# Kernel tuning notes

Hardware: AMD Instinct MI355X
Metric: run time of the kernel (lower is better)

The kernel has to match this reference:

```python
import jax, jax.numpy as jnp
import numpy as np
from jax import lax

L1_DECAY = 1e-06


def _maxpool2(x):
    # NCHW 2x2 max pool, stride 2
    return lax.reduce_window(x, -jnp.inf, lax.max, (1, 1, 2, 2), (1, 1, 2, 2), 'VALID')


def _cnn(x, w1, b1, w2, b2, wo, bo):
    # x: [N,128,128] -> [N,64], z-score normalized over batch dim
    x = x[:, None]  # [N,1,128,128]
    dn = ('NCHW', 'OIHW', 'NCHW')
    x = lax.conv_general_dilated(x, w1, (1, 1), 'SAME', dimension_numbers=dn) + b1[None, :, None, None]
    x = _maxpool2(jax.nn.relu(x))  # [N,4,64,64]
    x = lax.conv_general_dilated(x, w2, (1, 1), 'SAME', dimension_numbers=dn) + b2[None, :, None, None]
    x = _maxpool2(jax.nn.relu(x))  # [N,8,32,32]
    x = x.reshape(x.shape[0], -1)  # [N,8192] (C,H,W order, as torch .view)
    x = x @ wo.T + bo  # [N,64]
    mean = x.mean(axis=0)
    std = x.std(axis=0, ddof=1)  # torch unbiased std
    return (x - mean) / std


def _interact(item, nbr):
    # item: [N,64]; nbr: [N,H,K,64]. dot-attention over K per node/hop.
    scores = jnp.einsum('nhkd,nd->nhk', nbr, item)
    attn = jax.nn.softmax(scores, axis=-1)
    return jnp.einsum('nhk,nhkd->nhd', attn, nbr)  # [N,H,64]


def setup_inputs() -> dict:
    key = jax.random.key(0)
    ks = jax.random.split(key, 16)
    B = 4096
    inp = {}
    inp['data'] = jax.random.randint(ks[0], (B, 3), 0, 76)
    inp['cell_nbr'] = jax.random.randint(ks[1], (76, 2, 128), 0, 15970)
    inp['drug_nbr'] = jax.random.randint(ks[2], (764, 2, 128), 0, 15970)
    inp['protein_table'] = jax.random.normal(ks[3], (15970, 64), jnp.float32)
    inp['cell_emb_pre'] = jax.random.normal(ks[4], (76, 128, 128), jnp.float32)
    inp['drug_emb_pre'] = jax.random.normal(ks[5], (764, 128, 128), jnp.float32)
    inp['conv1_w'] = 0.05 * jax.random.normal(ks[6], (4, 1, 3, 3), jnp.float32)
    inp['conv1_b'] = 0.05 * jax.random.normal(ks[7], (4,), jnp.float32)
    inp['conv2_w'] = 0.05 * jax.random.normal(ks[8], (8, 4, 3, 3), jnp.float32)
    inp['conv2_b'] = 0.05 * jax.random.normal(ks[9], (8,), jnp.float32)
    inp['out_w'] = 0.05 * jax.random.normal(ks[10], (64, 8192), jnp.float32)
    inp['out_b'] = 0.05 * jax.random.normal(ks[11], (64,), jnp.float32)
    inp['agg_w'] = 0.05 * jax.random.normal(ks[12], (64, 128), jnp.float32)
    inp['agg_b'] = 0.05 * jax.random.normal(ks[13], (64,), jnp.float32)
    inp['comb_w'] = 0.05 * jax.random.normal(ks[14], (64, 128), jnp.float32)
    return inp


def reference(data, cell_nbr, drug_nbr, protein_table, cell_emb_pre, drug_emb_pre,
              conv1_w, conv1_b, conv2_w, conv2_b, out_w, out_b, agg_w, agg_b, comb_w):
    cells, drug1, drug2 = data[:, 0], data[:, 1], data[:, 2]
    B = data.shape[0]

    # per-node neighbor embedding gather: [num, n_hop, K, 64]
    cell_nbr_emb = protein_table[cell_nbr]
    drug_nbr_emb = protein_table[drug_nbr]

    # CNN item embeddings from precomputed images
    cell_item = _cnn(cell_emb_pre, conv1_w, conv1_b, conv2_w, conv2_b, out_w, out_b)  # [76,64]
    drug_item = _cnn(drug_emb_pre, conv1_w, conv1_b, conv2_w, conv2_b, out_w, out_b)  # [764,64]

    # gather -> attend -> weighted sum, then concat hops and aggregate
    cell_i = _interact(cell_item, cell_nbr_emb).reshape(cell_item.shape[0], -1)  # [76,128]
    drug_i = _interact(drug_item, drug_nbr_emb).reshape(drug_item.shape[0], -1)  # [764,128]
    cell_emb = cell_i @ agg_w.T + agg_b  # [76,64]
    drug_emb = drug_i @ agg_w.T + agg_b  # [764,64]

    # batch gather, keep singleton dim 1 to match torch stacking of [1,64]
    ce = cell_emb[cells][:, None, :]   # [B,1,64]
    d1e = drug_emb[drug1][:, None, :]
    d2e = drug_emb[drug2][:, None, :]

    # therapy: transformation_matrix
    combined = jnp.concatenate([d1e, d2e], axis=2) @ comb_w.T  # [B,1,64]
    therapy = (combined * ce).sum(axis=2)  # [B,1]
    toxic = (d1e * d2e).sum(axis=2)        # [B,1]
    score = therapy - toxic

    # emb loss (faithful to source: neighbor lists are indexed on the BATCH dim by hop)
    cnl = cell_nbr_emb[cells]   # [B,2,128,64]
    dnl1 = drug_nbr_emb[drug1]
    dnl2 = drug_nbr_emb[drug2]
    sq = lambda t: jnp.sum(t * t)
    item_reg = (sq(ce) + sq(d1e) + sq(d2e)) / 2
    node_reg = jnp.float32(0.0)
    for hop in range(2):
        node_reg = node_reg + (sq(cnl[hop]) + sq(dnl1[hop]) + sq(dnl2[hop])) / 2
    emb_loss = L1_DECAY * (item_reg + node_reg) / B
    return score, emb_loss
```

## Files before the change

### kernel.cpp

```cpp
#include <hip/hip_runtime.h>
#include <hip/hip_bf16.h>
#include <math.h>

#define N_CELL 76
#define N_DRUG 764
#define N_ITEM 840
#define BATCH  4096

#define POOL2H_B 0u
#define POOL2L_B 13762560u
#define WHI_B    27525120u
#define WLO_B    28573696u
#define XFC_B    29622272u
#define ITEM_B   29837312u
#define EMB_B    30052352u
#define V_B      30267392u
#define LOSS_B   30306304u
#define CNT_B    30306368u

typedef short bh8 __attribute__((ext_vector_type(8)));
typedef short bh4 __attribute__((ext_vector_type(4)));
typedef float f32x4 __attribute__((ext_vector_type(4)));

static __device__ inline unsigned short f2bf(float f) {
  union { float f; unsigned u; } v; v.f = f;
  unsigned r = v.u + 0x7FFFu + ((v.u >> 16) & 1u);
  return (unsigned short)(r >> 16);
}
static __device__ inline float bf2f(unsigned short h) {
  union { unsigned u; float f; } v; v.u = ((unsigned)h) << 16;
  return v.f;
}
static __device__ inline unsigned short f2bf_lo(float f, unsigned short h) {
  union { float f; unsigned u; } a; a.f = f - bf2f(h);
  return (unsigned short)(a.u >> 16);
}

union BH8U { bh8 v; struct { bh4 lo, hi; } s; };

__global__ __launch_bounds__(256) void k_conv12(
    const float* __restrict__ cell_pre, const float* __restrict__ drug_pre,
    const float* __restrict__ w1, const float* __restrict__ b1,
    const float* __restrict__ w2, const float* __restrict__ b2,
    const float* __restrict__ out_w,
    unsigned short* __restrict__ pool2h, unsigned short* __restrict__ pool2l,
    unsigned short* __restrict__ whi, unsigned short* __restrict__ wlo,
    float* __restrict__ xfc, float* __restrict__ loss, unsigned* __restrict__ cnt) {
  __shared__ unsigned short slh[38 * 34 * 4];
  __shared__ unsigned short sll[38 * 34 * 4];
  __shared__ unsigned short p1h[18 * 66 * 4];
  __shared__ unsigned short p1l[18 * 66 * 4];
  int n = blockIdx.y;
  int tid = threadIdx.x;
  if (n >= 840) {
    int cb = (n - 840) * 4 + blockIdx.x;
    int gid = cb * 256 + tid;
    if (gid == 0) { *loss = 0.f; *cnt = 0u; }
    for (int i = gid; i < 13440; i += 5120)
      ((float4*)xfc)[i] = make_float4(0.f, 0.f, 0.f, 0.f);
    for (int i = gid; i < 131072; i += 5120) {
      float4 v = ((const float4*)out_w)[i];
      ushort4 h, l;
      h.x = f2bf(v.x); l.x = f2bf(v.x - bf2f(h.x));
      h.y = f2bf(v.y); l.y = f2bf(v.y - bf2f(h.y));
      h.z = f2bf(v.z); l.z = f2bf(v.z - bf2f(h.z));
      h.w = f2bf(v.w); l.w = f2bf(v.w - bf2f(h.w));
      ((ushort4*)whi)[i] = h;
      ((ushort4*)wlo)[i] = l;
    }
    return;
  }
  int qt = blockIdx.x;
  const float4* src = (const float4*)((n < N_CELL) ? (cell_pre + (size_t)n * 16384)
                                                   : (drug_pre + (size_t)(n - N_CELL) * 16384));
  for (int i = tid; i < 38 * 32; i += 256) {
    int lr = i >> 5, g = i & 31;
    int iy = qt * 32 - 3 + lr;
    float4 v = make_float4(0.f, 0.f, 0.f, 0.f);
    if (iy >= 0 && iy < 128) v = src[iy * 32 + g];
    ushort4 h, l;
    h.x = f2bf(v.x); l.x = f2bf_lo(v.x, h.x);
    h.y = f2bf(v.y); l.y = f2bf_lo(v.y, h.y);
    h.z = f2bf(v.z); l.z = f2bf_lo(v.z, h.z);
    h.w = f2bf(v.w); l.w = f2bf_lo(v.w, h.w);
    ((ushort4*)slh)[lr * 34 + g + 1] = h;
    ((ushort4*)sll)[lr * 34 + g + 1] = l;
  }
  if (tid < 76) {
    int lr = tid >> 1, g = (tid & 1) ? 33 : 0;
    ushort4 z = make_ushort4(0, 0, 0, 0);
    ((ushort4*)slh)[lr * 34 + g] = z;
    ((ushort4*)sll)[lr * 34 + g] = z;
  }
  if (tid < 36) {
    int r = tid >> 1, c = (tid & 1) ? 65 : 0;
    ushort4 z = make_ushort4(0, 0, 0, 0);
    ((ushort4*)p1h)[r * 66 + c] = z;
    ((ushort4*)p1l)[r * 66 + c] = z;
  }
  int wv = tid >> 6;
  int lane = tid & 63;
  int ml = lane & 15, q = lane >> 4;

  int oc = ml & 3, yv1 = (ml >> 2) & 1, hi = ml >> 3;
  float bb = b1[oc];
  bh8 BhE, BlE, BhO, BlO;
  {
    int kr = q - yv1;
    bool krok = (kr >= 0 && kr <= 2);
#pragma unroll
    for (int j = 0; j < 8; ++j) {
      float ve = 0.f, vo = 0.f;
      if (krok) {
        int kse = j - 3 - 2 * hi;
        int kso = j - 2 * hi;
        if (kse >= 0 && kse <= 2) ve = w1[oc * 9 + kr * 3 + kse];
        if (kso >= 0 && kso <= 2) vo = w1[oc * 9 + kr * 3 + kso];
      }
      unsigned short he = f2bf(ve), ho = f2bf(vo);
      BhE[j] = (short)he; BlE[j] = (short)f2bf_lo(ve, he);
      BhO[j] = (short)ho; BlO[j] = (short)f2bf_lo(vo, ho);
    }
  }
  int oc_b = ml & 7, yv2 = ml >> 3;
  bh8 Bh2[2], Bl2[2];
#pragma unroll
  for (int ch = 0; ch < 2; ++ch) {
#pragma unroll
    for (int j = 0; j < 8; ++j) {
      int kg = ch * 32 + q * 8 + j;
      float v = 0.f;
      if (kg < 48) {
        int r = kg / 12, rem = kg - r * 12;
        int ks = rem >> 2, ic = rem & 3;
        int kr = r - yv2;
        if (kr >= 0 && kr <= 2) v = w2[(oc_b * 4 + ic) * 9 + kr * 3 + ks];
      } else if (kg == 48) {
        v = b2[oc_b];
      }
      unsigned short h = f2bf(v);
      Bh2[ch][j] = (short)h;
      Bl2[ch][j] = (short)f2bf_lo(v, h);
    }
  }
  int c0 = 2 * q, c1 = 2 * q + 1;
  int c2 = 8 + 2 * q, c3 = 9 + 2 * q;
  if (c2 > 11) { c2 = 8; c3 = 9; }
  int r0 = (c0 * 86) >> 8, s0 = c0 - 3 * r0;
  int r1 = (c1 * 86) >> 8, s1 = c1 - 3 * r1;
  int r2 = (c2 * 86) >> 8, s2 = c2 - 3 * r2;
  int r3 = (c3 * 86) >> 8, s3 = c3 - 3 * r3;
  int x2 = (wv & 3) << 4;
  int off0 = r0 * 66 + x2 + ml + s0;
  int off1 = r1 * 66 + x2 + ml + s1;
  int off2 = r2 * 66 + x2 + ml + s2;
  int off3 = r3 * 66 + x2 + ml + s3;
  __syncthreads();

  int x0 = (wv & 1) * 16;
  int rbase = (wv >> 1) * 9;
  int Lb = x0 + ml;
  const bh4* lh4 = (const bh4*)slh;
  const bh4* ll4 = (const bh4*)sll;
#pragma unroll 1
  for (int ii = 0; ii < 9; ++ii) {
    int i = rbase + ii;
    int base = (2 * i + q) * 34 + Lb;
    bh4 g0h = lh4[base], g1h = lh4[base + 1], g2h = lh4[base + 2];
    bh4 g0l = ll4[base], g1l = ll4[base + 1], g2l = ll4[base + 2];
    BH8U aeh, ael, aoh, aol;
    aeh.s.lo = g0h; aeh.s.hi = g1h;
    ael.s.lo = g0l; ael.s.hi = g1l;
    aoh.s.lo = g1h; aoh.s.hi = g2h;
    aol.s.lo = g1l; aol.s.hi = g2l;
    f32x4 de = {0.f, 0.f, 0.f, 0.f}, dd = de;
    de = __builtin_amdgcn_mfma_f32_16x16x32_bf16(aeh.v, BhE, de, 0, 0, 0);
    de = __builtin_amdgcn_mfma_f32_16x16x32_bf16(aeh.v, BlE, de, 0, 0, 0);
    de = __builtin_amdgcn_mfma_f32_16x16x32_bf16(ael.v, BhE, de, 0, 0, 0);
    dd = __builtin_amdgcn_mfma_f32_16x16x32_bf16(aoh.v, BhO, dd, 0, 0, 0);
    dd = __builtin_amdgcn_mfma_f32_16x16x32_bf16(aoh.v, BlO, dd, 0, 0, 0);
    dd = __builtin_amdgcn_mfma_f32_16x16x32_bf16(aol.v, BhO, dd, 0, 0, 0);
    int pr = qt * 16 - 1 + i;
    bool inr = (pr >= 0 && pr < 64);
#pragma unroll
    for (int r = 0; r < 4; ++r) {
      float t = fmaxf(de[r], dd[r]);
      float t2 = __shfl_xor(t, 4);
      if (yv1 == 0) {
        float val = fmaxf(fmaxf(t, t2) + bb, 0.f);
        if (!inr) val = 0.f;
        unsigned short h = f2bf(val);
        unsigned short l = f2bf_lo(val, h);
        int px = 2 * (x0 + q * 4 + r) + hi;
        int idx = (i * 66 + px + 1) * 4 + oc;
        p1h[idx] = h; p1l[idx] = l;
      }
    }
  }
  __syncthreads();

  const bh4* ph4 = (const bh4*)p1h;
  const bh4* pl4 = (const bh4*)p1l;
#pragma unroll 1
  for (int rp = 0; rp < 8; ++rp) {
    int base2 = 2 * rp * 66;
    BH8U ah0, al0, ah1, al1;
    ah0.s.lo = ph4[base2 + off0]; ah0.s.hi = ph4[base2 + off1];
    al0.s.lo = pl4[base2 + off0]; al0.s.hi = pl4[base2 + off1];
    if (q < 2) {
      ah1.s.lo = ph4[base2 + off2]; ah1.s.hi = ph4[base2 + off3];
      al1.s.lo = pl4[base2 + off2]; al1.s.hi = pl4[base2 + off3];
    } else {
#pragma unroll
      for (int j = 0; j < 8; ++j) { ah1.v[j] = 0; al1.v[j] = 0; }
      if (q == 2) ah1.v[0] = (short)0x3F80;
    }
    f32x4 accA = {0.f, 0.f, 0.f, 0.f}, accB = accA;
    accA = __builtin_amdgcn_mfma_f32_16x16x32_bf16(ah0.v, Bh2[0], accA, 0, 0, 0);
    accA = __builtin_amdgcn_mfma_f32_16x16x32_bf16(ah0.v, Bl2[0], accA, 0, 0, 0);
    accA = __builtin_amdgcn_mfma_f32_16x16x32_bf16(al0.v, Bh2[0], accA, 0, 0, 0);
    accB = __builtin_amdgcn_mfma_f32_16x16x32_bf16(ah1.v, Bh2[1], accB, 0, 0, 0);
    accB = __builtin_amdgcn_mfma_f32_16x16x32_bf16(ah1.v, Bl2[1], accB, 0, 0, 0);
    accB = __builtin_amdgcn_mfma_f32_16x16x32_bf16(al1.v, Bh2[1], accB, 0, 0, 0);
    float d0 = accA[0] + accB[0], d1 = accA[1] + accB[1];
    float d2 = accA[2] + accB[2], d3 = accA[3] + accB[3];
    float m0 = fmaxf(d0, d1), m1 = fmaxf(d2, d3);
    float o0 = __shfl_xor(m0, 8), o1 = __shfl_xor(m1, 8);
    m0 = fmaxf(fmaxf(m0, o0), 0.f);
    m1 = fmaxf(fmaxf(m1, o1), 0.f);
    if (yv2 == 0) {
      unsigned short h0 = f2bf(m0), h1 = f2bf(m1);
      unsigned short l0 = f2bf(m0 - bf2f(h0)), l1 = f2bf(m1 - bf2f(h1));
      int PR = qt * 8 + rp;
      unsigned ui = (unsigned)n * 4096u + (unsigned)oc_b * 512u +
                    (unsigned)PR * 16u + (unsigned)(x2 >> 2) + (unsigned)q;
      ((unsigned*)pool2h)[ui] = (unsigned)h0 | ((unsigned)h1 << 16);
      ((unsigned*)pool2l)[ui] = (unsigned)l0 | ((unsigned)l1 << 16);
    }
  }
}

__global__ __launch_bounds__(64) void k_fc(
    const unsigned short* __restrict__ pool2h, const unsigned short* __restrict__ pool2l,
    const unsigned short* __restrict__ whi, const unsigned short* __restrict__ wlo,
    float* __restrict__ xfc) {
  int mt = blockIdx.x, kc = blockIdx.y;
  int lane = threadIdx.x;
  int ml = lane & 15, q = lane >> 4;
  int row = mt * 16 + ml; if (row > N_ITEM - 1) row = N_ITEM - 1;
  size_t k0 = (size_t)kc * 256 + q * 8;
  const bh8* Ah = (const bh8*)(pool2h + (size_t)row * 8192 + k0);
  const bh8* Al = (const bh8*)(pool2l + (size_t)row * 8192 + k0);
  const bh8* Bh[4], * Bl[4];
#pragma unroll
  for (int nb = 0; nb < 4; ++nb) {
    Bh[nb] = (const bh8*)(whi + (size_t)(nb * 16 + ml) * 8192 + k0);
    Bl[nb] = (const bh8*)(wlo + (size_t)(nb * 16 + ml) * 8192 + k0);
  }
  f32x4 acc[4];
#pragma unroll
  for (int nb = 0; nb < 4; ++nb) acc[nb] = (f32x4){0.f, 0.f, 0.f, 0.f};
#pragma unroll
  for (int st = 0; st < 8; ++st) {
    bh8 ah = Ah[st * 4], al = Al[st * 4];
#pragma unroll
    for (int nb = 0; nb < 4; ++nb) {
      bh8 bhv = Bh[nb][st * 4], blv = Bl[nb][st * 4];
      acc[nb] = __builtin_amdgcn_mfma_f32_16x16x32_bf16(ah, bhv, acc[nb], 0, 0, 0);
      acc[nb] = __builtin_amdgcn_mfma_f32_16x16x32_bf16(ah, blv, acc[nb], 0, 0, 0);
      acc[nb] = __builtin_amdgcn_mfma_f32_16x16x32_bf16(al, bhv, acc[nb], 0, 0, 0);
    }
  }
#pragma unroll
  for (int r = 0; r < 4; ++r) {
    int mr = mt * 16 + q * 4 + r;
    if (mr < N_ITEM) {
      float* dst = xfc + (size_t)mr * 64 + ml;
#pragma unroll
      for (int nb = 0; nb < 4; ++nb) atomicAdd(dst + nb * 16, acc[nb][r]);
    }
  }
}

__global__ __launch_bounds__(256) void k_norm(
    const float* __restrict__ xfc, float* __restrict__ item) {
  __shared__ float red[256];
  int grp = blockIdx.x >> 6;
  int o = blockIdx.x & 63;
  int base = grp ? N_CELL : 0;
  int N = grp ? N_DRUG : N_CELL;
  int tid = threadIdx.x;
  float s = 0.f;
  for (int i = tid; i < N; i += 256) s += xfc[(size_t)(base + i) * 64 + o];
  red[tid] = s; __syncthreads();
  for (int w = 128; w > 0; w >>= 1) { if (tid < w) red[tid] += red[tid + w]; __syncthreads(); }
  float mean = red[0] / (float)N;
  __syncthreads();
  float sq = 0.f;
  for (int i = tid; i < N; i += 256) {
    float d = xfc[(size_t)(base + i) * 64 + o] - mean;
    sq += d * d;
  }
  red[tid] = sq; __syncthreads();
  for (int w = 128; w > 0; w >>= 1) { if (tid < w) red[tid] += red[tid + w]; __syncthreads(); }
  float inv_std = 1.f / sqrtf(red[0] / (float)(N - 1));
  for (int i = tid; i < N; i += 256)
    item[(size_t)(base + i) * 64 + o] = (xfc[(size_t)(base + i) * 64 + o] - mean) * inv_std;
}

__global__ __launch_bounds__(256) void k_interact(
    const int* __restrict__ cell_nbr, const int* __restrict__ drug_nbr,
    const float* __restrict__ protein, const float* __restrict__ item,
    const float* __restrict__ agg_w, const float* __restrict__ agg_b,
    const float* __restrict__ comb_w, float* __restrict__ emb,
    float* __restrict__ V) {
  __shared__ float pb[128 * 65];
  __shared__ float item_s[64];
  __shared__ float sc[128];
  __shared__ float hop_out[128];
  __shared__ float red[256];
  __shared__ float emb_f[64];
  int n = blockIdx.x;
  int tid = threadIdx.x;
  const int* nbr = (n < N_CELL) ? (cell_nbr + (size_t)n * 256)
                                : (drug_nbr + (size_t)(n - N_CELL) * 256);
  if (tid < 64) item_s[tid] = item[(size_t)n * 64 + tid];
  __syncthreads();
  for (int h = 0; h < 2; ++h) {
    for (int e = tid; e < 8192; e += 256) {
      int k = e >> 6, d = e & 63;
      int idx = nbr[h * 128 + k];
      pb[k * 65 + d] = protein[(size_t)idx * 64 + d];
    }
    __syncthreads();
    {
      int k = tid >> 1, halfd = tid & 1;
      int d0 = halfd * 32;
      float p = 0.f;
#pragma unroll
      for (int d = 0; d < 32; ++d) p += item_s[d0 + d] * pb[k * 65 + d0 + d];
      p += __shfl_xor(p, 1);
      if (halfd == 0) sc[k] = p;
    }
    __syncthreads();
    if (tid < 64) {
      float a = sc[tid], b = sc[tid + 64];
      float m = fmaxf(a, b);
#pragma unroll
      for (int off = 32; off > 0; off >>= 1) m = fmaxf(m, __shfl_xor(m, off));
      float e0 = __expf(a - m), e1 = __expf(b - m);
      float s = e0 + e1;
#pragma unroll
      for (int off = 32; off > 0; off >>= 1) s += __shfl_xor(s, off);
      float inv = 1.f / s;
      sc[tid] = e0 * inv; sc[tid + 64] = e1 * inv;
    }
    __syncthreads();
    {
      int d = tid & 63, kq = tid >> 6;
      float p = 0.f;
#pragma unroll
      for (int k = 0; k < 32; ++k) {
        int kk = kq * 32 + k;
        p += sc[kk] * pb[kk * 65 + d];
      }
      red[tid] = p;
    }
    __syncthreads();
    if (tid < 64)
      hop_out[h * 64 + tid] = red[tid] + red[tid + 64] + red[tid + 128] + red[tid + 192];
    __syncthreads();
  }
  {
    int o = tid & 63, jq = tid >> 6;
    float p = 0.f;
#pragma unroll
    for (int j = 0; j < 32; ++j) {
      int jj = jq * 32 + j;
      p += hop_out[jj] * agg_w[(size_t)o * 128 + jj];
    }
    red[tid] = p;
  }
  __syncthreads();
  if (tid < 64) {
    float ev = red[tid] + red[tid + 64] + red[tid + 128] + red[tid + 192] + agg_b[tid];
    emb[(size_t)n * 64 + tid] = ev;
    emb_f[tid] = ev;
  }
  if (n < N_CELL) {
    __syncthreads();
    if (tid < 128) {
      float s = 0.f;
#pragma unroll
      for (int o = 0; o < 64; ++o) s += comb_w[(size_t)o * 128 + tid] * emb_f[o];
      V[(size_t)n * 128 + tid] = s;
    }
  }
}

__global__ __launch_bounds__(256) void k_scoreall(
    const int* __restrict__ data, const int* __restrict__ cell_nbr,
    const int* __restrict__ drug_nbr, const float* __restrict__ protein,
    const float* __restrict__ emb, const float* __restrict__ V,
    float* __restrict__ out, float* __restrict__ loss, unsigned* __restrict__ cnt) {
  __shared__ float red[256];
  int bx = blockIdx.x;
  int tid = threadIdx.x;
  if (bx < 1024) {
    int lane = tid & 63;
    int w = tid >> 6;
    int b = bx * 4 + w;
    int c = data[b * 3 + 0], d1 = data[b * 3 + 1], d2 = data[b * 3 + 2];
    float ce = emb[(size_t)c * 64 + lane];
    float e1 = emb[(size_t)(N_CELL + d1) * 64 + lane];
    float e2 = emb[(size_t)(N_CELL + d2) * 64 + lane];
    float v1 = V[(size_t)c * 128 + lane];
    float v2 = V[(size_t)c * 128 + 64 + lane];
    float th = e1 * v1 + e2 * v2;
    float tx = e1 * e2;
    float rg = ce * ce + e1 * e1 + e2 * e2;
#pragma unroll
    for (int off = 32; off > 0; off >>= 1) {
      th += __shfl_xor(th, off);
      tx += __shfl_xor(tx, off);
      rg += __shfl_xor(rg, off);
    }
    if (lane == 0) { out[b] = th - tx; red[w] = rg; }
    __syncthreads();
    if (tid == 0) atomicAdd(loss, 0.5f * (red[0] + red[1] + red[2] + red[3]));
  } else {
    int j = bx - 1024;
    int hop = j / 3, which = j % 3;
    int row = data[hop * 3 + which];
    const int* nbr = (which == 0) ? (cell_nbr + (size_t)row * 256)
                                  : (drug_nbr + (size_t)row * 256);
    float acc = 0.f;
    for (int e = tid; e < 16384; e += 256) {
      int k = e >> 6, d = e & 63;
      float v = protein[(size_t)nbr[k] * 64 + d];
      acc += v * v;
    }
    red[tid] = acc; __syncthreads();
    for (int w = 128; w > 0; w >>= 1) { if (tid < w) red[tid] += red[tid + w]; __syncthreads(); }
    if (tid == 0) atomicAdd(loss, 0.5f * red[0]);
  }
  if (tid == 0) {
    __threadfence();
    unsigned old = atomicAdd(cnt, 1u);
    if (old == gridDim.x - 1) {
      float L = atomicAdd(loss, 0.f);
      out[BATCH] = L * (1e-6f / 4096.f);
    }
  }
}

extern "C" void kernel_launch(void* const* d_in, const int* in_sizes, int n_in,
                              void* d_out, int out_size, void* d_ws, size_t ws_size,
                              hipStream_t stream) {
  const int*   data      = (const int*)d_in[0];
  const int*   cell_nbr  = (const int*)d_in[1];
  const int*   drug_nbr  = (const int*)d_in[2];
  const float* protein   = (const float*)d_in[3];
  const float* cell_pre  = (const float*)d_in[4];
  const float* drug_pre  = (const float*)d_in[5];
  const float* w1        = (const float*)d_in[6];
  const float* b1        = (const float*)d_in[7];
  const float* w2        = (const float*)d_in[8];
  const float* b2        = (const float*)d_in[9];
  const float* out_w     = (const float*)d_in[10];
  const float* agg_w     = (const float*)d_in[12];
  const float* agg_b     = (const float*)d_in[13];
  const float* comb_w    = (const float*)d_in[14];
  float* out = (float*)d_out;
  char* base = (char*)d_ws;
  unsigned short* pool2h  = (unsigned short*)(base + POOL2H_B);
  unsigned short* pool2l  = (unsigned short*)(base + POOL2L_B);
  unsigned short* whi     = (unsigned short*)(base + WHI_B);
  unsigned short* wlo     = (unsigned short*)(base + WLO_B);
  float* xfc              = (float*)(base + XFC_B);
  float* item             = (float*)(base + ITEM_B);
  float* emb              = (float*)(base + EMB_B);
  float* V                = (float*)(base + V_B);
  float* loss             = (float*)(base + LOSS_B);
  unsigned* cnt           = (unsigned*)(base + CNT_B);

  k_conv12<<<dim3(4, 845), 256, 0, stream>>>(cell_pre, drug_pre, w1, b1, w2, b2, out_w,
                                             pool2h, pool2l, whi, wlo, xfc, loss, cnt);
  k_fc<<<dim3(53, 32), 64, 0, stream>>>(pool2h, pool2l, whi, wlo, xfc);
  k_norm<<<128, 256, 0, stream>>>(xfc, item);
  k_interact<<<840, 256, 0, stream>>>(cell_nbr, drug_nbr, protein, item, agg_w, agg_b,
                                      comb_w, emb, V);
  k_scoreall<<<1030, 256, 0, stream>>>(data, cell_nbr, drug_nbr, protein, emb, V, out, loss, cnt);
}
```

Before: 253.2 us.

## Double block size in conv and interact kernels, splitting rows and hops across waves

Raises k_conv12 and k_interact from 256 to 512 threads per block. In conv, the conv1 row loop is split across 8 waves with uneven 5/4-row ranges, and the conv2 row-pair loop is halved per wave. In interact, the two hops run at the same time on the two thread halves, each with its own shared buffer, which removes the sequential hop loop and its barriers. This costs roughly double the LDS per interact block and may lower occupancy. The hidden conv code must stay consistent with the new wave indexing.

```diff
diff --git a/kernel.cpp b/kernel.cpp
--- a/kernel.cpp
+++ b/kernel.cpp
@@ -38,7 +38,7 @@
 
 union BH8U { bh8 v; struct { bh4 lo, hi; } s; };
 
-__global__ __launch_bounds__(256) void k_conv12(
+__global__ __launch_bounds__(512) void k_conv12(
     const float* __restrict__ cell_pre, const float* __restrict__ drug_pre,
     const float* __restrict__ w1, const float* __restrict__ b1,
     const float* __restrict__ w2, const float* __restrict__ b2,
@@ -54,11 +54,11 @@
   int tid = threadIdx.x;
   if (n >= 840) {
     int cb = (n - 840) * 4 + blockIdx.x;
-    int gid = cb * 256 + tid;
+    int gid = cb * 512 + tid;
     if (gid == 0) { *loss = 0.f; *cnt = 0u; }
-    for (int i = gid; i < 13440; i += 5120)
+    for (int i = gid; i < 13440; i += 10240)
       ((float4*)xfc)[i] = make_float4(0.f, 0.f, 0.f, 0.f);
-    for (int i = gid; i < 131072; i += 5120) {
+    for (int i = gid; i < 131072; i += 10240) {
       float4 v = ((const float4*)out_w)[i];
       ushort4 h, l;
       h.x = f2bf(v.x); l.x = f2bf(v.x - bf2f(h.x));
@@ -73,7 +73,7 @@
   int qt = blockIdx.x;
   const float4* src = (const float4*)((n < N_CELL) ? (cell_pre + (size_t)n * 16384)
                                                    : (drug_pre + (size_t)(n - N_CELL) * 16384));
-  for (int i = tid; i < 38 * 32; i += 256) {
+  for (int i = tid; i < 38 * 32; i += 512) {
     int lr = i >> 5, g = i & 31;
     int iy = qt * 32 - 3 + lr;
     float4 v = make_float4(0.f, 0.f, 0.f, 0.f);
@@ -158,12 +158,14 @@
   __syncthreads();
 
   int x0 = (wv & 1) * 16;
-  int rbase = (wv >> 1) * 9;
+  int g1 = wv >> 1;
+  int rbase = (g1 < 2) ? g1 * 5 : 10 + (g1 - 2) * 4;
+  int rcnt  = (g1 < 2) ? 5 : 4;
   int Lb = x0 + ml;
   const bh4* lh4 = (const bh4*)slh;
   const bh4* ll4 = (const bh4*)sll;
 #pragma unroll 1
-  for (int ii = 0; ii < 9; ++ii) {
+  for (int ii = 0; ii < rcnt; ++ii) {
     int i = rbase + ii;
     int base = (2 * i + q) * 34 + Lb;
     bh4 g0h = lh4[base], g1h = lh4[base + 1], g2h = lh4[base + 2];
@@ -199,10 +201,12 @@
   }
   __syncthreads();
 
+  int rp0 = (wv >> 2) * 4;
   const bh4* ph4 = (const bh4*)p1h;
   const bh4* pl4 = (const bh4*)p1l;
 #pragma unroll 1
-  for (int rp = 0; rp < 8; ++rp) {
+  for (int rr = 0; rr < 4; ++rr) {
+    int rp = rp0 + rr;
     int base2 = 2 * rp * 66;
     BH8U ah0, al0, ah1, al1;
     ah0.s.lo = ph4[base2 + off0]; ah0.s.hi = ph4[base2 + off1];
@@ -308,82 +312,85 @@
     item[(size_t)(base + i) * 64 + o] = (xfc[(size_t)(base + i) * 64 + o] - mean) * inv_std;
 }
 
-__global__ __launch_bounds__(256) void k_interact(
+__global__ __launch_bounds__(512) void k_interact(
     const int* __restrict__ cell_nbr, const int* __restrict__ drug_nbr,
     const float* __restrict__ protein, const float* __restrict__ item,
     const float* __restrict__ agg_w, const float* __restrict__ agg_b,
     const float* __restrict__ comb_w, float* __restrict__ emb,
     float* __restrict__ V) {
-  __shared__ float pb[128 * 65];
+  __shared__ float pb[2][128 * 65];
   __shared__ float item_s[64];
-  __shared__ float sc[128];
+  __shared__ float sc[2][128];
   __shared__ float hop_out[128];
-  __shared__ float red[256];
+  __shared__ float red[512];
   __shared__ float emb_f[64];
   int n = blockIdx.x;
   int tid = threadIdx.x;
+  int ht = tid >> 8;
+  int t = tid & 255;
   const int* nbr = (n < N_CELL) ? (cell_nbr + (size_t)n * 256)
                                 : (drug_nbr + (size_t)(n - N_CELL) * 256);
   if (tid < 64) item_s[tid] = item[(size_t)n * 64 + tid];
   __syncthreads();
-  for (int h = 0; h < 2; ++h) {
-    for (int e = tid; e < 8192; e += 256) {
-      int k = e >> 6, d = e & 63;
-      int idx = nbr[h * 128 + k];
-      pb[k * 65 + d] = protein[(size_t)idx * 64 + d];
-    }
-    __syncthreads();
-    {
-      int k = tid >> 1, halfd = tid & 1;
-      int d0 = halfd * 32;
-      float p = 0.f;
-#pragma unroll
-      for (int d = 0; d < 32; ++d) p += item_s[d0 + d] * pb[k * 65 + d0 + d];
-      p += __shfl_xor(p, 1);
-      if (halfd == 0) sc[k] = p;
-    }
-    __syncthreads();
-    if (tid < 64) {
-      float a = sc[tid], b = sc[tid + 64];
-      float m = fmaxf(a, b);
-#pragma unroll
-      for (int off = 32; off > 0; off >>= 1) m = fmaxf(m, __shfl_xor(m, off));
-      float e0 = __expf(a - m), e1 = __expf(b - m);
-      float s = e0 + e1;
-#pragma unroll
-      for (int off = 32; off > 0; off >>= 1) s += __shfl_xor(s, off);
-      float inv = 1.f / s;
-      sc[tid] = e0 * inv; sc[tid + 64] = e1 * inv;
-    }
-    __syncthreads();
-    {
-      int d = tid & 63, kq = tid >> 6;
-      float p = 0.f;
-#pragma unroll
-      for (int k = 0; k < 32; ++k) {
-        int kk = kq * 32 + k;
-        p += sc[kk] * pb[kk * 65 + d];
-      }
-      red[tid] = p;
-    }
-    __syncthreads();
-    if (tid < 64)
-      hop_out[h * 64 + tid] = red[tid] + red[tid + 64] + red[tid + 128] + red[tid + 192];
-    __syncthreads();
-  }
+  for (int e = t; e < 8192; e += 256) {
+    int k = e >> 6, d = e & 63;
+    int idx = nbr[ht * 128 + k];
+    pb[ht][k * 65 + d] = protein[(size_t)idx * 64 + d];
+  }
+  __syncthreads();
+  {
+    int k = t >> 1, halfd = t & 1;
+    int d0 = halfd * 32;
+    float p = 0.f;
+#pragma unroll
+    for (int d = 0; d < 32; ++d) p += item_s[d0 + d] * pb[ht][k * 65 + d0 + d];
+    p += __shfl_xor(p, 1);
+    if (halfd == 0) sc[ht][k] = p;
+  }
+  __syncthreads();
+  if (t < 64) {
+    float a = sc[ht][t], b = sc[ht][t + 64];
+    float m = fmaxf(a, b);
+#pragma unroll
+    for (int off = 32; off > 0; off >>= 1) m = fmaxf(m, __shfl_xor(m, off));
+    float e0 = __expf(a - m), e1 = __expf(b - m);
+    float s = e0 + e1;
+#pragma unroll
+    for (int off = 32; off > 0; off >>= 1) s += __shfl_xor(s, off);
+    float inv = 1.f / s;
+    sc[ht][t] = e0 * inv; sc[ht][t + 64] = e1 * inv;
+  }
+  __syncthreads();
+  {
+    int d = t & 63, kq = t >> 6;
+    float p = 0.f;
+#pragma unroll
+    for (int k = 0; k < 32; ++k) {
+      int kk = kq * 32 + k;
+      p += sc[ht][kk] * pb[ht][kk * 65 + d];
+    }
+    red[tid] = p;
+  }
+  __syncthreads();
+  if (t < 64)
+    hop_out[ht * 64 + t] = red[ht * 256 + t] + red[ht * 256 + t + 64] +
+                           red[ht * 256 + t + 128] + red[ht * 256 + t + 192];
+  __syncthreads();
   {
     int o = tid & 63, jq = tid >> 6;
     float p = 0.f;
 #pragma unroll
-    for (int j = 0; j < 32; ++j) {
-      int jj = jq * 32 + j;
+    for (int j = 0; j < 16; ++j) {
+      int jj = jq * 16 + j;
       p += hop_out[jj] * agg_w[(size_t)o * 128 + jj];
     }
     red[tid] = p;
   }
   __syncthreads();
   if (tid < 64) {
-    float ev = red[tid] + red[tid + 64] + red[tid + 128] + red[tid + 192] + agg_b[tid];
+    float ev = red[tid] + red[tid + 64] + red[tid + 128] + red[tid + 192] +
+               red[tid + 256] + red[tid + 320] + red[tid + 384] + red[tid + 448] +
+               agg_b[tid];
     emb[(size_t)n * 64 + tid] = ev;
     emb_f[tid] = ev;
   }
@@ -484,11 +491,11 @@
   float* loss             = (float*)(base + LOSS_B);
   unsigned* cnt           = (unsigned*)(base + CNT_B);
 
-  k_conv12<<<dim3(4, 845), 256, 0, stream>>>(cell_pre, drug_pre, w1, b1, w2, b2, out_w,
+  k_conv12<<<dim3(4, 845), 512, 0, stream>>>(cell_pre, drug_pre, w1, b1, w2, b2, out_w,
                                              pool2h, pool2l, whi, wlo, xfc, loss, cnt);
   k_fc<<<dim3(53, 32), 64, 0, stream>>>(pool2h, pool2l, whi, wlo, xfc);
   k_norm<<<128, 256, 0, stream>>>(xfc, item);
-  k_interact<<<840, 256, 0, stream>>>(cell_nbr, drug_nbr, protein, item, agg_w, agg_b,
+  k_interact<<<840, 512, 0, stream>>>(cell_nbr, drug_nbr, protein, item, agg_w, agg_b,
                                       comb_w, emb, V);
   k_scoreall<<<1030, 256, 0, stream>>>(data, cell_nbr, drug_nbr, protein, emb, V, out, loss, cnt);
 }
```

Result: no change. 251.3 us (-0.7%).
